# Performance work log

Measured on AMD Instinct MI355X. Metric: run time of the kernel, lower is better.

Reference implementation:

```python
import jax, jax.numpy as jnp
import numpy as np

HIDDEN = 1024
HEAD_DIM = 64
N_EXPERTS = 16
MIN_EXPERTS = 2
B, T = 4, 2048


def _normalize(x, axis):
    # matches torch.nn.functional.normalize (L2, eps=1e-12)
    n = jnp.sqrt(jnp.sum(x * x, axis=axis, keepdims=True))
    return x / jnp.maximum(n, 1e-12)


def _ste(x):
    # straight-through: forward = (x > 0), backward = identity
    hard = jax.lax.stop_gradient((x > 0).astype(x.dtype))
    return hard + x - jax.lax.stop_gradient(x)


def setup_inputs() -> dict:
    key = jax.random.key(0)
    ks = jax.random.split(key, 6)
    xav_qkv = float(np.sqrt(6.0 / (HIDDEN + HEAD_DIM)))
    return {
        "hidden_states": jax.random.normal(ks[0], (B, T, HIDDEN), dtype=jnp.float32),
        "sim_matrix": jax.random.normal(ks[1], (HIDDEN, N_EXPERTS), dtype=jnp.float32),
        "gates": jnp.zeros((N_EXPERTS,), dtype=jnp.float32),
        "q_proj": jax.random.uniform(ks[2], (N_EXPERTS, HIDDEN, HEAD_DIM), jnp.float32, -xav_qkv, xav_qkv),
        "k_proj": jax.random.uniform(ks[3], (N_EXPERTS, HIDDEN, HEAD_DIM), jnp.float32, -xav_qkv, xav_qkv),
        "v_proj": jax.random.uniform(ks[4], (N_EXPERTS, HIDDEN, HEAD_DIM), jnp.float32, -xav_qkv, xav_qkv),
        "o_proj": jax.random.uniform(ks[5], (N_EXPERTS, HEAD_DIM, HIDDEN), jnp.float32, -xav_qkv, xav_qkv),
    }


def _gating(hidden_states, sim_matrix, gates):
    b, t, c = hidden_states.shape
    flat = hidden_states.reshape(b * t, c)
    logits = _normalize(flat, -1) @ _normalize(sim_matrix, 0) - jax.nn.sigmoid(gates)
    gated = jax.nn.relu(logits)
    mask = _ste(gated)
    inactive = jnp.sum(mask, axis=1) == 0  # (b*t,)
    # top-min_experts fallback for fully-inactive tokens
    _, fb_idx = jax.lax.top_k(logits, MIN_EXPERTS)
    fb = jnp.zeros_like(mask).at[jnp.arange(b * t)[:, None], fb_idx].set(1.0)
    fb_applied = inactive[:, None] & (fb > 0)
    mask = jnp.where(fb_applied, 1.0, mask)
    masked_logits = jnp.where(mask > 0, gated, -jnp.inf)
    return jax.nn.softmax(masked_logits, axis=-1).reshape(b, t, -1)


def reference(hidden_states, sim_matrix, gates, q_proj, k_proj, v_proj, o_proj):
    b, t, c = hidden_states.shape
    rw = _gating(hidden_states, sim_matrix, gates)  # (b,t,E)
    # per-expert GEMM then weighted reduction over E (same math as the
    # original 'bte,ecd->btdc' / 'btc,btdc->btd' chain, without the btdc tensor)
    q = jnp.einsum("bte,bted->btd", rw, jnp.einsum("btc,ecd->bted", hidden_states, q_proj))
    k = jnp.einsum("bte,bted->btd", rw, jnp.einsum("btc,ecd->bted", hidden_states, k_proj))
    v = jnp.einsum("bte,bted->btd", rw, jnp.einsum("btc,ecd->bted", hidden_states, v_proj))
    # single-head causal SDPA
    scale = 1.0 / jnp.sqrt(jnp.asarray(HEAD_DIM, dtype=q.dtype))
    scores = jnp.einsum("bqd,bkd->bqk", q, k) * scale
    causal = jnp.tril(jnp.ones((t, t), dtype=bool))
    scores = jnp.where(causal, scores, -jnp.inf)
    attn = jnp.einsum("bqk,bkd->bqd", jax.nn.softmax(scores, axis=-1), v)
    # output projection: weight attn per expert, then expert GEMM
    mixed = attn[:, :, None, :] * rw[..., None]  # (b,t,E,d)
    return jnp.einsum("bted,edc->btc", mixed, o_proj)
```

## Files before the change

kernel.cpp:

```cpp
#include <hip/hip_runtime.h>
#include <math.h>

#define HIDDEN 1024
#define HEAD_DIM 64
#define NEXP 16
#define NTOK 8192
#define SEQ 2048
#define NB 4

#define OFF_PREP   0
#define OFF_CNT    256
#define OFF_TOK    512
#define OFF_WGT    (OFF_TOK + 524288)
#define OFF_RW     (OFF_WGT + 524288)
#define OFF_Q      (OFF_RW + 524288)
#define OFF_K      (OFF_Q + 2097152)
#define OFF_V      (OFF_K + 2097152)
#define OFF_ATTN   (OFF_V + 2097152)
#define OFF_ACCP   (OFF_ATTN + 2097152)
#define OFF_MLP    (OFF_ACCP + 8388608)
#define WS_NEED_SPLIT (OFF_MLP + 262144)

__global__ __launch_bounds__(256) void prep_kernel(const float* __restrict__ sim,
                                                   const float* __restrict__ gates,
                                                   float* __restrict__ prep) {
    int tid = threadIdx.x;
    int e = tid & 15, part = tid >> 4;
    float ss = 0.f;
    for (int c = part; c < HIDDEN; c += 16) {
        float v = sim[c * NEXP + e];
        ss += v * v;
    }
    __shared__ float red[16][17];
    red[part][e] = ss;
    __syncthreads();
    if (tid < 16) {
        float s = 0.f;
        #pragma unroll
        for (int p = 0; p < 16; ++p) s += red[p][tid];
        prep[tid] = 1.f / fmaxf(sqrtf(s), 1e-12f);
        prep[16 + tid] = 1.f / (1.f + expf(-gates[tid]));
    }
}

__global__ __launch_bounds__(256) void gating_kernel(const float* __restrict__ h,
                                                     const float* __restrict__ sim,
                                                     const float* __restrict__ prep,
                                                     int* __restrict__ counts,
                                                     int* __restrict__ tok_list,
                                                     float* __restrict__ wgt_list,
                                                     float* __restrict__ rw_dense) {
    int t = blockIdx.x;
    int tid = threadIdx.x;
    const float* hrow = h + (size_t)t * HIDDEN;
    float dot[16];
    #pragma unroll
    for (int e = 0; e < 16; ++e) dot[e] = 0.f;
    float ss = 0.f;
    for (int c = tid; c < HIDDEN; c += 256) {
        float hv = hrow[c];
        ss += hv * hv;
        const float4* s4 = (const float4*)(sim + c * NEXP);
        float4 a = s4[0], b = s4[1], cc = s4[2], d = s4[3];
        dot[0]  += hv * a.x;  dot[1]  += hv * a.y;  dot[2]  += hv * a.z;  dot[3]  += hv * a.w;
        dot[4]  += hv * b.x;  dot[5]  += hv * b.y;  dot[6]  += hv * b.z;  dot[7]  += hv * b.w;
        dot[8]  += hv * cc.x; dot[9]  += hv * cc.y; dot[10] += hv * cc.z; dot[11] += hv * cc.w;
        dot[12] += hv * d.x;  dot[13] += hv * d.y;  dot[14] += hv * d.z;  dot[15] += hv * d.w;
    }
    int lane = tid & 63, wv = tid >> 6;
    #pragma unroll
    for (int off = 32; off > 0; off >>= 1) {
        ss += __shfl_down(ss, off, 64);
        #pragma unroll
        for (int e = 0; e < 16; ++e) dot[e] += __shfl_down(dot[e], off, 64);
    }
    __shared__ float red[4][17];
    if (lane == 0) {
        red[wv][16] = ss;
        #pragma unroll
        for (int e = 0; e < 16; ++e) red[wv][e] = dot[e];
    }
    __syncthreads();
    if (tid == 0) {
        float tss = 0.f;
        float td[16];
        #pragma unroll
        for (int e = 0; e < 16; ++e) td[e] = 0.f;
        for (int w = 0; w < 4; ++w) {
            tss += red[w][16];
            #pragma unroll
            for (int e = 0; e < 16; ++e) td[e] += red[w][e];
        }
        float invh = 1.f / fmaxf(sqrtf(tss), 1e-12f);
        float logits[16], gated[16];
        bool mask[16];
        int nact = 0;
        #pragma unroll
        for (int e = 0; e < 16; ++e) {
            logits[e] = td[e] * invh * prep[e] - prep[16 + e];
            gated[e] = fmaxf(logits[e], 0.f);
            mask[e] = logits[e] > 0.f;
            if (mask[e]) nact++;
        }
        if (nact == 0) {
            int i1 = 0; float v1 = logits[0];
            for (int e = 1; e < 16; ++e) if (logits[e] > v1) { v1 = logits[e]; i1 = e; }
            int i2 = -1; float v2 = -INFINITY;
            for (int e = 0; e < 16; ++e) if (e != i1 && logits[e] > v2) { v2 = logits[e]; i2 = e; }
            mask[i1] = true; mask[i2] = true;
        }
        float m = -INFINITY;
        #pragma unroll
        for (int e = 0; e < 16; ++e) if (mask[e]) m = fmaxf(m, gated[e]);
        float sum = 0.f;
        float p[16];
        #pragma unroll
        for (int e = 0; e < 16; ++e) {
            p[e] = mask[e] ? expf(gated[e] - m) : 0.f;
            sum += p[e];
        }
        float inv = 1.f / sum;
        for (int e = 0; e < 16; ++e) {
            if (mask[e]) {
                float w = p[e] * inv;
                rw_dense[(size_t)t * 16 + e] = w;
                int pos = atomicAdd(&counts[e], 1);
                tok_list[e * NTOK + pos] = t;
                wgt_list[e * NTOK + pos] = w;
            } else {
                rw_dense[(size_t)t * 16 + e] = 0.f;
            }
        }
    }
}

__global__ __launch_bounds__(256) void expert_qkv_v5(const float* __restrict__ h,
                                                     const float* __restrict__ qw,
                                                     const float* __restrict__ kw,
                                                     const float* __restrict__ vw,
                                                     const int* __restrict__ counts,
                                                     const int* __restrict__ tok_list,
                                                     const float* __restrict__ wgt_list,
                                                     float* __restrict__ qb,
                                                     float* __restrict__ kb,
                                                     float* __restrict__ vb) {
    int bid = blockIdx.x;
    int e = bid >> 7, chunk = (bid >> 1) & 63, ks = bid & 1;
    int cnt = counts[e];
    int base = chunk * 128;
    if (base >= cnt) return;
    const float* W0 = qw + (size_t)e * HIDDEN * HEAD_DIM;
    const float* W1 = kw + (size_t)e * HIDDEN * HEAD_DIM;
    const float* W2 = vw + (size_t)e * HIDDEN * HEAD_DIM;

    __shared__ int s_tok[128];
    __shared__ float s_wt[128];
    __shared__ float h_s[128][20];
    __shared__ float w_s[3][16][68];
    int tid = threadIdx.x;
    if (tid < 128) {
        int idx = base + tid;
        s_tok[tid] = idx < cnt ? tok_list[e * NTOK + idx] : -1;
        s_wt[tid] = idx < cnt ? wgt_list[e * NTOK + idx] : 0.f;
    }
    __syncthreads();
    int tokl = tid >> 1, hf = (tid & 1) * 8;
    int tg = tid >> 4, dg = tid & 15;
    int tok_stage = s_tok[tokl];
    const float* hrow = h + (size_t)(tok_stage >= 0 ? tok_stage : 0) * HIDDEN;

    float acc[3][8][4];
    #pragma unroll
    for (int tt = 0; tt < 3; ++tt)
        #pragma unroll
        for (int i = 0; i < 8; ++i)
            #pragma unroll
            for (int j = 0; j < 4; ++j) acc[tt][i][j] = 0.f;

    int widx0 = tid, widx1 = 256 + tid, widx2 = 512 + tid;

    int koff = ks * 512;
    float4 ph0 = make_float4(0.f, 0.f, 0.f, 0.f), ph1 = ph0;
    if (tok_stage >= 0) {
        ph0 = *(const float4*)&hrow[koff + hf];
        ph1 = *(const float4*)&hrow[koff + hf + 4];
    }
    float4 pw[3];
    {
        int idxs[3] = {widx0, widx1, widx2};
        #pragma unroll
        for (int r = 0; r < 3; ++r) {
            int tt = idxs[r] >> 8, rem = idxs[r] & 255;
            int k = rem >> 4, c4 = (rem & 15) * 4;
            const float* Wt = tt == 0 ? W0 : tt == 1 ? W1 : W2;
            pw[r] = *(const float4*)&Wt[(size_t)(koff + k) * HEAD_DIM + c4];
        }
    }

    for (int kt = 0; kt < 32; ++kt) {
        __syncthreads();
        *(float4*)&h_s[tokl][hf] = ph0;
        *(float4*)&h_s[tokl][hf + 4] = ph1;
        {
            int idxs[3] = {widx0, widx1, widx2};
            #pragma unroll
            for (int r = 0; r < 3; ++r) {
                int tt = idxs[r] >> 8, rem = idxs[r] & 255;
                int k = rem >> 4, c4 = (rem & 15) * 4;
                *(float4*)&w_s[tt][k][c4] = pw[r];
            }
        }
        __syncthreads();
        if (kt < 31) {
            int kn = koff + (kt + 1) * 16;
            if (tok_stage >= 0) {
                ph0 = *(const float4*)&hrow[kn + hf];
                ph1 = *(const float4*)&hrow[kn + hf + 4];
            }
            int idxs[3] = {widx0, widx1, widx2};
            #pragma unroll
            for (int r = 0; r < 3; ++r) {
                int tt = idxs[r] >> 8, rem = idxs[r] & 255;
                int k = rem >> 4, c4 = (rem & 15) * 4;
                const float* Wt = tt == 0 ? W0 : tt == 1 ? W1 : W2;
                pw[r] = *(const float4*)&Wt[(size_t)(kn + k) * HEAD_DIM + c4];
            }
        }
        #pragma unroll
        for (int kq = 0; kq < 4; ++kq) {
            float4 h4[8];
            #pragma unroll
            for (int i = 0; i < 8; ++i) h4[i] = *(float4*)&h_s[tg * 8 + i][kq * 4];
            #pragma unroll
            for (int kk = 0; kk < 4; ++kk) {
                int k2 = kq * 4 + kk;
                float4 b0 = *(float4*)&w_s[0][k2][dg * 4];
                float4 b1 = *(float4*)&w_s[1][k2][dg * 4];
                float4 b2 = *(float4*)&w_s[2][k2][dg * 4];
                #pragma unroll
                for (int i = 0; i < 8; ++i) {
                    float a = (kk == 0) ? h4[i].x : (kk == 1) ? h4[i].y : (kk == 2) ? h4[i].z : h4[i].w;
                    acc[0][i][0] += a * b0.x; acc[0][i][1] += a * b0.y; acc[0][i][2] += a * b0.z; acc[0][i][3] += a * b0.w;
                    acc[1][i][0] += a * b1.x; acc[1][i][1] += a * b1.y; acc[1][i][2] += a * b1.z; acc[1][i][3] += a * b1.w;
                    acc[2][i][0] += a * b2.x; acc[2][i][1] += a * b2.y; acc[2][i][2] += a * b2.z; acc[2][i][3] += a * b2.w;
                }
            }
        }
    }
    #pragma unroll
    for (int i = 0; i < 8; ++i) {
        int r = tg * 8 + i;
        int tok = s_tok[r];
        if (tok >= 0) {
            float wgt = s_wt[r];
            size_t off = (size_t)tok * HEAD_DIM + dg * 4;
            #pragma unroll
            for (int j = 0; j < 4; ++j) {
                atomicAdd(&qb[off + j], wgt * acc[0][i][j]);
                atomicAdd(&kb[off + j], wgt * acc[1][i][j]);
                atomicAdd(&vb[off + j], wgt * acc[2][i][j]);
            }
        }
    }
}

__global__ __launch_bounds__(256) void attn_split(const float* __restrict__ q,
                                                  const float* __restrict__ k,
                                                  const float* __restrict__ v,
                                                  float* __restrict__ o,
                                                  float* __restrict__ accp,
                                                  float* __restrict__ mlp,
                                                  int nchunks) {
    int b = blockIdx.z;
    int c = blockIdx.y;
    int q0 = blockIdx.x * 32;
    int cw = (nchunks == 1) ? SEQ : 512;
    int kbeg = c * cw;
    if (kbeg > q0) return;
    int kend = min(kbeg + cw, q0 + 32);
    int nkt = (kend - kbeg) >> 5;

    int tid = threadIdx.x;
    int r = tid >> 3, g = tid & 7;
    int qg = q0 + r;

    __shared__ float k_s[32][68];
    __shared__ float v_s[32][68];

    float4 qv[16];
    const float* qrow = q + ((size_t)(b * SEQ + qg)) * HEAD_DIM;
    #pragma unroll
    for (int i = 0; i < 16; ++i) qv[i] = *(const float4*)(qrow + i * 4);

    float acc[8];
    #pragma unroll
    for (int i = 0; i < 8; ++i) acc[i] = 0.f;
    float m = -INFINITY, l = 0.f;

    const float* kp = k + ((size_t)(b * SEQ + kbeg + r)) * HEAD_DIM + g * 8;
    const float* vp = v + ((size_t)(b * SEQ + kbeg + r)) * HEAD_DIM + g * 8;
    float4 pk0 = *(const float4*)kp,       pk1 = *(const float4*)(kp + 4);
    float4 pv0 = *(const float4*)vp,       pv1 = *(const float4*)(vp + 4);

    for (int kt = 0; kt < nkt; ++kt) {
        __syncthreads();
        *(float4*)&k_s[r][g * 8] = pk0;  *(float4*)&k_s[r][g * 8 + 4] = pk1;
        *(float4*)&v_s[r][g * 8] = pv0;  *(float4*)&v_s[r][g * 8 + 4] = pv1;
        __syncthreads();
        if (kt + 1 < nkt) {
            const float* kn = kp + (size_t)(kt + 1) * 32 * HEAD_DIM;
            const float* vn = vp + (size_t)(kt + 1) * 32 * HEAD_DIM;
            pk0 = *(const float4*)kn; pk1 = *(const float4*)(kn + 4);
            pv0 = *(const float4*)vn; pv1 = *(const float4*)(vn + 4);
        }
        float s[4] = {0.f, 0.f, 0.f, 0.f};
        #pragma unroll
        for (int d4 = 0; d4 < 16; ++d4) {
            float4 a = qv[d4];
            #pragma unroll
            for (int j = 0; j < 4; ++j) {
                float4 kk4 = *(float4*)&k_s[g * 4 + j][d4 * 4];
                s[j] += a.x * kk4.x + a.y * kk4.y + a.z * kk4.z + a.w * kk4.w;
            }
        }
        float pm = -INFINITY;
        #pragma unroll
        for (int j = 0; j < 4; ++j) {
            int key = kbeg + kt * 32 + g * 4 + j;
            s[j] = (key <= qg) ? s[j] * 0.125f : -INFINITY;
            pm = fmaxf(pm, s[j]);
        }
        pm = fmaxf(pm, __shfl_xor(pm, 1, 64));
        pm = fmaxf(pm, __shfl_xor(pm, 2, 64));
        pm = fmaxf(pm, __shfl_xor(pm, 4, 64));
        float mnew = fmaxf(m, pm);
        float corr = __expf(m - mnew);
        float p[4];
        float psum = 0.f;
        #pragma unroll
        for (int j = 0; j < 4; ++j) {
            p[j] = __expf(s[j] - mnew);
            psum += p[j];
        }
        psum += __shfl_xor(psum, 1, 64);
        psum += __shfl_xor(psum, 2, 64);
        psum += __shfl_xor(psum, 4, 64);
        l = l * corr + psum;
        m = mnew;
        #pragma unroll
        for (int d = 0; d < 8; ++d) acc[d] *= corr;
        #pragma unroll
        for (int kk = 0; kk < 32; ++kk) {
            float pb = __shfl(p[kk & 3], (r << 3) | (kk >> 2), 64);
            float4 v0 = *(float4*)&v_s[kk][g * 8];
            float4 v1 = *(float4*)&v_s[kk][g * 8 + 4];
            acc[0] += pb * v0.x; acc[1] += pb * v0.y; acc[2] += pb * v0.z; acc[3] += pb * v0.w;
            acc[4] += pb * v1.x; acc[5] += pb * v1.y; acc[6] += pb * v1.z; acc[7] += pb * v1.w;
        }
    }

    if (nchunks == 1) {
        float invl = 1.f / l;
        float* orow = o + ((size_t)(b * SEQ + qg)) * HEAD_DIM + g * 8;
        *(float4*)orow = make_float4(acc[0] * invl, acc[1] * invl, acc[2] * invl, acc[3] * invl);
        *(float4*)(orow + 4) = make_float4(acc[4] * invl, acc[5] * invl, acc[6] * invl, acc[7] * invl);
    } else {
        size_t pidx = ((size_t)(c * NB + b) * SEQ + qg);
        float* arow = accp + pidx * HEAD_DIM + g * 8;
        *(float4*)arow = make_float4(acc[0], acc[1], acc[2], acc[3]);
        *(float4*)(arow + 4) = make_float4(acc[4], acc[5], acc[6], acc[7]);
        if (g == 0) { mlp[pidx * 2] = m; mlp[pidx * 2 + 1] = l; }
    }
}

__global__ __launch_bounds__(256) void attn_combine(const float* __restrict__ accp,
                                                    const float* __restrict__ mlp,
                                                    float* __restrict__ o) {
    int gr = blockIdx.x * 4 + (threadIdx.x >> 6);
    int d = threadIdx.x & 63;
    int b = gr >> 11, row = gr & 2047;
    int nact = (row >> 9) + 1;
    float M = -INFINITY;
    for (int c = 0; c < nact; ++c)
        M = fmaxf(M, mlp[(((size_t)(c * NB + b) * SEQ) + row) * 2]);
    float L = 0.f, A = 0.f;
    for (int c = 0; c < nact; ++c) {
        size_t pidx = ((size_t)(c * NB + b) * SEQ) + row;
        float ec = __expf(mlp[pidx * 2] - M);
        L += mlp[pidx * 2 + 1] * ec;
        A += accp[pidx * HEAD_DIM + d] * ec;
    }
    o[((size_t)(b * SEQ) + row) * HEAD_DIM + d] = A / L;
}

__global__ __launch_bounds__(256) void expert_out_v2(const float* __restrict__ attn,
                                                     const float* __restrict__ ow,
                                                     const float* __restrict__ rw_dense,
                                                     float* __restrict__ out) {
    int t0 = blockIdx.x * 64;
    int c0 = blockIdx.y * 64;
    int tid = threadIdx.x;

    __shared__ float x_s[64][68];
    __shared__ float o_s[64][68];
    __shared__ float acc_s[64][68];
    __shared__ float rw_s[64][16];
    __shared__ int lst[64];
    __shared__ int lcnt;

    #pragma unroll
    for (int r = 0; r < 4; ++r) {
        int idx = r * 256 + tid;
        int t = idx >> 4, q = idx & 15;
        *(float4*)&x_s[t][q * 4] = *(const float4*)&attn[(size_t)(t0 + t) * HEAD_DIM + q * 4];
        *(float4*)&acc_s[t][q * 4] = make_float4(0.f, 0.f, 0.f, 0.f);
    }
    {
        int t = tid >> 2, eg = tid & 3;
        *(float4*)&rw_s[t][eg * 4] = *(const float4*)&rw_dense[(size_t)(t0 + t) * 16 + eg * 4];
    }
    __syncthreads();

    for (int e = 0; e < 16; ++e) {
        if (tid == 0) lcnt = 0;
        __syncthreads();
        if (tid < 64 && rw_s[tid][e] != 0.f) {
            int p = atomicAdd(&lcnt, 1);
            lst[p] = tid;
        }
        #pragma unroll
        for (int r = 0; r < 4; ++r) {
            int idx = r * 256 + tid;
            int d = idx >> 4, q = idx & 15;
            *(float4*)&o_s[d][q * 4] =
                *(const float4*)&ow[(size_t)e * HEAD_DIM * HIDDEN + (size_t)d * HIDDEN + c0 + q * 4];
        }
        __syncthreads();
        int P = lcnt;
        int pg = tid >> 4, c4 = (tid & 15) * 4;
        for (int p = pg; p < P; p += 16) {
            int t = lst[p];
            float w = rw_s[t][e];
            float sx = 0.f, sy = 0.f, sz = 0.f, sw = 0.f;
            #pragma unroll 8
            for (int d = 0; d < 64; ++d) {
                float xv = x_s[t][d];
                float4 o4 = *(float4*)&o_s[d][c4];
                sx += xv * o4.x; sy += xv * o4.y; sz += xv * o4.z; sw += xv * o4.w;
            }
            float4 a = *(float4*)&acc_s[t][c4];
            a.x += w * sx; a.y += w * sy; a.z += w * sz; a.w += w * sw;
            *(float4*)&acc_s[t][c4] = a;
        }
        __syncthreads();
    }
    #pragma unroll
    for (int r = 0; r < 4; ++r) {
        int idx = r * 256 + tid;
        int t = idx >> 4, q = idx & 15;
        *(float4*)&out[(size_t)(t0 + t) * HIDDEN + c0 + q * 4] = *(float4*)&acc_s[t][q * 4];
    }
}

extern "C" void kernel_launch(void* const* d_in, const int* in_sizes, int n_in,
                              void* d_out, int out_size, void* d_ws, size_t ws_size,
                              hipStream_t stream) {
    const float* h     = (const float*)d_in[0];
    const float* sim   = (const float*)d_in[1];
    const float* gates = (const float*)d_in[2];
    const float* qw    = (const float*)d_in[3];
    const float* kw    = (const float*)d_in[4];
    const float* vw    = (const float*)d_in[5];
    const float* ow    = (const float*)d_in[6];
    float* out = (float*)d_out;

    char* w = (char*)d_ws;
    float* prep     = (float*)(w + OFF_PREP);
    int*   counts   = (int*)(w + OFF_CNT);
    int*   tok_list = (int*)(w + OFF_TOK);
    float* wgt_list = (float*)(w + OFF_WGT);
    float* rw_dense = (float*)(w + OFF_RW);
    float* qb       = (float*)(w + OFF_Q);
    float* kb       = (float*)(w + OFF_K);
    float* vb       = (float*)(w + OFF_V);
    float* attnb    = (float*)(w + OFF_ATTN);
    float* accp     = (float*)(w + OFF_ACCP);
    float* mlp      = (float*)(w + OFF_MLP);

    hipMemsetAsync(counts, 0, 64, stream);
    hipMemsetAsync(qb, 0, 3 * 2097152, stream);

    prep_kernel<<<1, 256, 0, stream>>>(sim, gates, prep);
    gating_kernel<<<NTOK, 256, 0, stream>>>(h, sim, prep, counts, tok_list, wgt_list, rw_dense);
    expert_qkv_v5<<<16 * 64 * 2, 256, 0, stream>>>(h, qw, kw, vw, counts, tok_list, wgt_list,
                                                   qb, kb, vb);
    if (ws_size >= (size_t)WS_NEED_SPLIT) {
        attn_split<<<dim3(64, 4, NB), 256, 0, stream>>>(qb, kb, vb, attnb, accp, mlp, 4);
        attn_combine<<<2048, 256, 0, stream>>>(accp, mlp, attnb);
    } else {
        attn_split<<<dim3(64, 1, NB), 256, 0, stream>>>(qb, kb, vb, attnb, attnb, attnb, 1);
    }
    expert_out_v2<<<dim3(128, 16), 256, 0, stream>>>(attnb, ow, rw_dense, out);
}
```

Measured before the change: 764.7 us.

## Run expert QKV projection on bf16 MFMA with pre-transposed bf16 weights

New measurement: 618.4 us. 1.24x faster.

```diff
diff --git a/kernel.cpp b/kernel.cpp
--- a/kernel.cpp
+++ b/kernel.cpp
@@ -7,6 +7,9 @@
 #define NTOK 8192
 #define SEQ 2048
 #define NB 4
+
+typedef short bf16x8 __attribute__((ext_vector_type(8)));
+typedef float f32x4 __attribute__((ext_vector_type(4)));
 
 #define OFF_PREP   0
 #define OFF_CNT    256
@@ -20,6 +23,13 @@
 #define OFF_ACCP   (OFF_ATTN + 2097152)
 #define OFF_MLP    (OFF_ACCP + 8388608)
 #define WS_NEED_SPLIT (OFF_MLP + 262144)
+#define OFF_WT     OFF_ACCP
+
+__device__ __forceinline__ unsigned short f2bf(float x) {
+    unsigned u = __builtin_bit_cast(unsigned, x);
+    unsigned r = (u + 0x7FFFu + ((u >> 16) & 1u)) >> 16;
+    return (unsigned short)r;
+}
 
 __global__ __launch_bounds__(256) void prep_kernel(const float* __restrict__ sim,
                                                    const float* __restrict__ gates,
@@ -129,6 +139,169 @@
                 wgt_list[e * NTOK + pos] = w;
             } else {
                 rw_dense[(size_t)t * 16 + e] = 0.f;
+            }
+        }
+    }
+}
+
+__global__ __launch_bounds__(256) void wt_convert(const float* __restrict__ qw,
+                                                  const float* __restrict__ kw,
+                                                  const float* __restrict__ vw,
+                                                  unsigned short* __restrict__ wt) {
+    int b = blockIdx.x;
+    int tt = b >> 7, e = (b >> 3) & 15, kt = b & 7;
+    const float* W = (tt == 0 ? qw : tt == 1 ? kw : vw) + (size_t)e * HIDDEN * HEAD_DIM;
+    __shared__ unsigned short kd[128][68];
+    int tid = threadIdx.x;
+    #pragma unroll
+    for (int u = 0; u < 8; ++u) {
+        int flat = u * 256 + tid;
+        int k = flat >> 4, d4 = (flat & 15) * 4;
+        float4 w4 = *(const float4*)&W[(size_t)(kt * 128 + k) * HEAD_DIM + d4];
+        unsigned short b0 = f2bf(w4.x), b1 = f2bf(w4.y), b2 = f2bf(w4.z), b3 = f2bf(w4.w);
+        unsigned int p0 = (unsigned int)b0 | ((unsigned int)b1 << 16);
+        unsigned int p1 = (unsigned int)b2 | ((unsigned int)b3 << 16);
+        *(unsigned int*)&kd[k][d4] = p0;
+        *(unsigned int*)&kd[k][d4 + 2] = p1;
+    }
+    __syncthreads();
+    unsigned short* wrow = wt + ((size_t)(tt * 16 + e) * HEAD_DIM) * HIDDEN + (size_t)kt * 128;
+    #pragma unroll
+    for (int u = 0; u < 4; ++u) {
+        int flat = u * 256 + tid;
+        int d = flat >> 4, k8 = (flat & 15) * 8;
+        unsigned int pk[4];
+        #pragma unroll
+        for (int j = 0; j < 4; ++j) {
+            unsigned int lo = kd[k8 + 2 * j][d];
+            unsigned int hi = kd[k8 + 2 * j + 1][d];
+            pk[j] = lo | (hi << 16);
+        }
+        *(uint4*)&wrow[(size_t)d * HIDDEN + k8] = make_uint4(pk[0], pk[1], pk[2], pk[3]);
+    }
+}
+
+__global__ __launch_bounds__(256) void expert_qkv_v6(const float* __restrict__ h,
+                                                     const unsigned short* __restrict__ wt,
+                                                     const int* __restrict__ counts,
+                                                     const int* __restrict__ tok_list,
+                                                     const float* __restrict__ wgt_list,
+                                                     float* __restrict__ qb,
+                                                     float* __restrict__ kb,
+                                                     float* __restrict__ vb) {
+    int e = blockIdx.x >> 7, chunk = blockIdx.x & 127;
+    int cnt = counts[e];
+    int base = chunk * 64;
+    if (base >= cnt) return;
+
+    __shared__ int s_tok[64];
+    __shared__ float s_wt[64];
+    __shared__ __align__(16) unsigned short h_s[64][72];
+    __shared__ __align__(16) unsigned short wt_s[3][64][72];
+
+    int tid = threadIdx.x;
+    int lane = tid & 63, wv = tid >> 6;
+    if (tid < 64) {
+        int idx = base + tid;
+        s_tok[tid] = idx < cnt ? tok_list[e * NTOK + idx] : -1;
+        s_wt[tid] = idx < cnt ? wgt_list[e * NTOK + idx] : 0.f;
+    }
+    __syncthreads();
+
+    int stok = tid >> 2, skq = (tid & 3) * 16;
+    int tok_stage = s_tok[stok];
+    const float* hrow = h + (size_t)(tok_stage >= 0 ? tok_stage : 0) * HIDDEN;
+    const unsigned short* wbase = wt + (size_t)e * HEAD_DIM * HIDDEN;
+
+    f32x4 acc[3][4];
+    #pragma unroll
+    for (int tt = 0; tt < 3; ++tt)
+        #pragma unroll
+        for (int mt = 0; mt < 4; ++mt)
+            acc[tt][mt] = (f32x4){0.f, 0.f, 0.f, 0.f};
+
+    float4 ph[4];
+    uint4 pwt[6];
+    {
+        #pragma unroll
+        for (int r = 0; r < 4; ++r) {
+            ph[r] = make_float4(0.f, 0.f, 0.f, 0.f);
+            if (tok_stage >= 0) ph[r] = *(const float4*)&hrow[skq + r * 4];
+        }
+        #pragma unroll
+        for (int i = 0; i < 6; ++i) {
+            int flat = i * 256 + tid;
+            int ttx = flat >> 9, rem = flat & 511;
+            int d = rem >> 3, k8 = (rem & 7) * 8;
+            pwt[i] = *(const uint4*)&wbase[((size_t)ttx * 16 * HEAD_DIM + d) * HIDDEN + k8];
+        }
+    }
+
+    for (int step = 0; step < 16; ++step) {
+        __syncthreads();
+        {
+            unsigned int pk[8];
+            const float* f = (const float*)ph;
+            #pragma unroll
+            for (int j = 0; j < 8; ++j)
+                pk[j] = (unsigned int)f2bf(f[2 * j]) | ((unsigned int)f2bf(f[2 * j + 1]) << 16);
+            *(uint4*)&h_s[stok][skq] = make_uint4(pk[0], pk[1], pk[2], pk[3]);
+            *(uint4*)&h_s[stok][skq + 8] = make_uint4(pk[4], pk[5], pk[6], pk[7]);
+        }
+        #pragma unroll
+        for (int i = 0; i < 6; ++i) {
+            int flat = i * 256 + tid;
+            int ttx = flat >> 9, rem = flat & 511;
+            int d = rem >> 3, k8 = (rem & 7) * 8;
+            *(uint4*)&wt_s[ttx][d][k8] = pwt[i];
+        }
+        __syncthreads();
+        if (step < 15) {
+            int koff = (step + 1) * 64;
+            #pragma unroll
+            for (int r = 0; r < 4; ++r) {
+                if (tok_stage >= 0) ph[r] = *(const float4*)&hrow[koff + skq + r * 4];
+            }
+            #pragma unroll
+            for (int i = 0; i < 6; ++i) {
+                int flat = i * 256 + tid;
+                int ttx = flat >> 9, rem = flat & 511;
+                int d = rem >> 3, k8 = (rem & 7) * 8;
+                pwt[i] = *(const uint4*)&wbase[((size_t)ttx * 16 * HEAD_DIM + d) * HIDDEN + koff + k8];
+            }
+        }
+        #pragma unroll
+        for (int ks = 0; ks < 2; ++ks) {
+            int kf = ks * 32 + (lane >> 4) * 8;
+            bf16x8 a[4], bfr[3];
+            #pragma unroll
+            for (int mt = 0; mt < 4; ++mt)
+                a[mt] = *(const bf16x8*)&h_s[mt * 16 + (lane & 15)][kf];
+            #pragma unroll
+            for (int tt = 0; tt < 3; ++tt)
+                bfr[tt] = *(const bf16x8*)&wt_s[tt][wv * 16 + (lane & 15)][kf];
+            #pragma unroll
+            for (int tt = 0; tt < 3; ++tt)
+                #pragma unroll
+                for (int mt = 0; mt < 4; ++mt)
+                    acc[tt][mt] = __builtin_amdgcn_mfma_f32_16x16x32_bf16(a[mt], bfr[tt],
+                                                                          acc[tt][mt], 0, 0, 0);
+        }
+    }
+
+    int dcol = wv * 16 + (lane & 15);
+    #pragma unroll
+    for (int mt = 0; mt < 4; ++mt) {
+        #pragma unroll
+        for (int r = 0; r < 4; ++r) {
+            int rl = mt * 16 + (lane >> 4) * 4 + r;
+            int tok = s_tok[rl];
+            if (tok >= 0) {
+                float wgt = s_wt[rl];
+                size_t off = (size_t)tok * HEAD_DIM + dcol;
+                atomicAdd(&qb[off], wgt * acc[0][mt][r]);
+                atomicAdd(&kb[off], wgt * acc[1][mt][r]);
+                atomicAdd(&vb[off], wgt * acc[2][mt][r]);
             }
         }
     }
@@ -178,7 +351,6 @@
             for (int j = 0; j < 4; ++j) acc[tt][i][j] = 0.f;
 
     int widx0 = tid, widx1 = 256 + tid, widx2 = 512 + tid;
-
     int koff = ks * 512;
     float4 ph0 = make_float4(0.f, 0.f, 0.f, 0.f), ph1 = ph0;
     if (tok_stage >= 0) {
@@ -486,15 +658,24 @@
     float* attnb    = (float*)(w + OFF_ATTN);
     float* accp     = (float*)(w + OFF_ACCP);
     float* mlp      = (float*)(w + OFF_MLP);
+    unsigned short* wtb = (unsigned short*)(w + OFF_WT);
 
     hipMemsetAsync(counts, 0, 64, stream);
     hipMemsetAsync(qb, 0, 3 * 2097152, stream);
 
     prep_kernel<<<1, 256, 0, stream>>>(sim, gates, prep);
     gating_kernel<<<NTOK, 256, 0, stream>>>(h, sim, prep, counts, tok_list, wgt_list, rw_dense);
-    expert_qkv_v5<<<16 * 64 * 2, 256, 0, stream>>>(h, qw, kw, vw, counts, tok_list, wgt_list,
-                                                   qb, kb, vb);
-    if (ws_size >= (size_t)WS_NEED_SPLIT) {
+
+    bool big_ws = ws_size >= (size_t)WS_NEED_SPLIT;
+    if (big_ws) {
+        wt_convert<<<384, 256, 0, stream>>>(qw, kw, vw, wtb);
+        expert_qkv_v6<<<16 * 128, 256, 0, stream>>>(h, wtb, counts, tok_list, wgt_list,
+                                                    qb, kb, vb);
+    } else {
+        expert_qkv_v5<<<16 * 64 * 2, 256, 0, stream>>>(h, qw, kw, vw, counts, tok_list,
+                                                       wgt_list, qb, kb, vb);
+    }
+    if (big_ws) {
         attn_split<<<dim3(64, 4, NB), 256, 0, stream>>>(qb, kb, vb, attnb, accp, mlp, 4);
         attn_combine<<<2048, 256, 0, stream>>>(accp, mlp, attnb);
     } else {
```
